# Kernel tuning notes

Hardware: AMD Instinct MI355X
Metric: run time of the kernel (lower is better)

## Reference

```python
import jax, jax.numpy as jnp
import numpy as np

BINS = 32
MAX_DIST = 128
EMB = 1024
DQ = 64
DV = 64
H = 16
B = 8
L = 1024


def _t5_bucket_table():
    # matches: clamp(n,max=m) + (log(clamp(n,min=m)-m+1)*(bins-1-m)/log(max_distance-m+1)).long()
    n = np.arange(MAX_DIST + 1)
    m = BINS // 2
    idx = np.minimum(n, m) + (
        np.log(np.maximum(n, m) - m + 1) * (BINS - 1 - m) / np.log(MAX_DIST - m + 1)
    ).astype(np.int64)
    return jnp.asarray(idx)


def setup_inputs() -> dict:
    key = jax.random.key(0)
    ks = jax.random.split(key, 8)
    s = 0.02
    return {
        "x": jax.random.normal(ks[0], (B, L, EMB), dtype=jnp.float32),
        "qk_w": jax.random.normal(ks[1], (2 * DQ * H, EMB), dtype=jnp.float32) * s,
        "qk_b": jnp.zeros((2 * DQ * H,), dtype=jnp.float32),
        "v_w": jax.random.normal(ks[2], (DV * H, EMB), dtype=jnp.float32) * s,
        "v_b": jnp.zeros((DV * H,), dtype=jnp.float32),
        "out_w": jax.random.normal(ks[3], (EMB, DV * H), dtype=jnp.float32) * s,
        "out_b": jnp.zeros((EMB,), dtype=jnp.float32),
        "bias": jax.random.normal(ks[4], (BINS, H), dtype=jnp.float32) * s,  # causal -> bins rows
    }


def reference(x, qk_w, qk_b, v_w, v_b, out_w, out_b, bias):
    # projections
    qk = (x @ qk_w.T + qk_b).reshape(B, L, H, 2 * DQ).transpose(0, 2, 1, 3)  # [B,H,L,2DQ]
    q, k = qk[..., :DQ], qk[..., DQ:]
    v = (x @ v_w.T + v_b).reshape(B, L, H, DV).transpose(0, 2, 1, 3)  # [B,H,L,DV]

    # T5 relative-position bias (causal): gather per (i-j) distance bucket
    idx_tab = _t5_bucket_table()
    shifts = jnp.arange(L)[:, None] - jnp.arange(L)[None, :]  # [L,L], i - j
    bins_idx = idx_tab[jnp.clip(jnp.abs(shifts), 0, MAX_DIST)]  # [L,L]
    bmat = bias[bins_idx].transpose(2, 0, 1)  # [H,L,L]
    bmat = jnp.where(shifts < 0, -jnp.inf, bmat)  # causal mask (j > i)

    scale = 1.0 / np.sqrt(DQ).astype(np.float32)
    scores = jnp.einsum("bhid,bhjd->bhij", q, k) * scale + bmat  # [B,H,L,L]
    attn = jax.nn.softmax(scores, axis=-1)
    out = jnp.einsum("bhij,bhjd->bhid", attn, v)  # [B,H,L,DV]
    out = out.transpose(0, 2, 1, 3).reshape(B, L, H * DV)
    return out @ out_w.T + out_b
```

## Files before the change

kernel.cpp:

```cpp
#include <hip/hip_runtime.h>
#include <cmath>


typedef _Float16 f16x8 __attribute__((ext_vector_type(8)));
typedef _Float16 f16x4 __attribute__((ext_vector_type(4)));
typedef float    f32x4 __attribute__((ext_vector_type(4)));

#define NEG_INF (-__builtin_inff())
#define LOG2E 1.4426950408889634f

#if __has_builtin(__builtin_amdgcn_exp2f)
#define EXP2(x) __builtin_amdgcn_exp2f(x)
#else
#define EXP2(x) exp2f(x)
#endif

__device__ __forceinline__ void gl_lds16(const void* g, void* l) {
  __builtin_amdgcn_global_load_lds(
      (__attribute__((address_space(1))) void*)g,
      (__attribute__((address_space(3))) void*)l,
      16, 0, 0);
}

__device__ __forceinline__ f32x4 mfma32(f16x8 a, f16x8 b, f32x4 c) {
  return __builtin_amdgcn_mfma_f32_16x16x32_f16(a, b, c, 0, 0, 0);
}
__device__ __forceinline__ f32x4 mfma16(f16x4 a, f16x4 b, f32x4 c) {
  return __builtin_amdgcn_mfma_f32_16x16x16f16(a, b, c, 0, 0, 0);
}

__global__ void cvt_kernel(const float* __restrict__ in,
                           _Float16* __restrict__ out, int n4) {
  int i = blockIdx.x * blockDim.x + threadIdx.x;
  if (i >= n4) return;
  float4 v = reinterpret_cast<const float4*>(in)[i];
  f16x4 o;
  o[0] = (_Float16)v.x; o[1] = (_Float16)v.y;
  o[2] = (_Float16)v.z; o[3] = (_Float16)v.w;
  reinterpret_cast<f16x4*>(out)[i] = o;
}

template <int MODE>
__global__ __launch_bounds__(256, 4) void gemm_kernel(
    const _Float16* __restrict__ A, const _Float16* __restrict__ Bm,
    int M, int N, int K,
    const float* __restrict__ bias_q, const float* __restrict__ bias_v,
    _Float16* __restrict__ qkbuf, _Float16* __restrict__ vtbuf,
    const float* __restrict__ bias_o, float* __restrict__ outf) {
  __shared__ __align__(16) _Float16 lds_a[2][128 * 32];
  __shared__ __align__(16) _Float16 lds_b[2][128 * 32];
  const int t = threadIdx.x;
  const int w = t >> 6;
  const int lane = t & 63;
  const int lq = lane & 15, lg = lane >> 4;
  const int wr = w >> 1, wc = w & 1;
  const int m0 = blockIdx.y * 128, n0 = blockIdx.x * 128;

  const _Float16* pA0 = A + (size_t)(m0 + (t >> 2)) * K + (t & 3) * 8;
  const _Float16* pA1 = pA0 + (size_t)64 * K;
  const _Float16* pB0 = Bm + (size_t)(n0 + (t >> 2)) * K + (t & 3) * 8;
  const _Float16* pB1 = pB0 + (size_t)64 * K;
  const int wofs = w * 512;

#define GEMM_STAGE(buf, kk)                      \
  do {                                           \
    gl_lds16(pA0 + (kk), &lds_a[buf][wofs]);     \
    gl_lds16(pA1 + (kk), &lds_a[buf][2048 + wofs]); \
    gl_lds16(pB0 + (kk), &lds_b[buf][wofs]);     \
    gl_lds16(pB1 + (kk), &lds_b[buf][2048 + wofs]); \
  } while (0)

#define GEMM_COMPUTE(buf)                                                    \
  do {                                                                       \
    f16x8 af[4], bfr[4];                                                     \
    _Pragma("unroll") for (int mi = 0; mi < 4; ++mi) af[mi] =                \
        *(const f16x8*)&lds_a[buf][(wr * 64 + mi * 16 + lq) * 32 + lg * 8];  \
    _Pragma("unroll") for (int ni = 0; ni < 4; ++ni) bfr[ni] =               \
        *(const f16x8*)&lds_b[buf][(wc * 64 + ni * 16 + lq) * 32 + lg * 8];  \
    __builtin_amdgcn_s_setprio(1);                                           \
    _Pragma("unroll") for (int mi = 0; mi < 4; ++mi)                         \
        _Pragma("unroll") for (int ni = 0; ni < 4; ++ni) acc[mi][ni] =       \
            mfma32(af[mi], bfr[ni], acc[mi][ni]);                            \
    __builtin_amdgcn_s_setprio(0);                                           \
  } while (0)

  f32x4 acc[4][4];
#pragma unroll
  for (int mi = 0; mi < 4; ++mi)
#pragma unroll
    for (int ni = 0; ni < 4; ++ni) acc[mi][ni] = (f32x4){0.f, 0.f, 0.f, 0.f};

  GEMM_STAGE(0, 0);

  int cur = 0;
  for (int k0 = 0; k0 < K - 32; k0 += 32) {
    const int nx = cur ^ 1;
    GEMM_STAGE(nx, k0 + 32);
    asm volatile("s_waitcnt vmcnt(4)" ::: "memory");
    __builtin_amdgcn_s_barrier();
    asm volatile("" ::: "memory");
    GEMM_COMPUTE(cur);
    asm volatile("" ::: "memory");
    __builtin_amdgcn_s_barrier();
    cur = nx;
  }
  asm volatile("s_waitcnt vmcnt(0)" ::: "memory");
  __builtin_amdgcn_s_barrier();
  asm volatile("" ::: "memory");
  GEMM_COMPUTE(cur);
#undef GEMM_STAGE
#undef GEMM_COMPUTE

  if (MODE == 0) {
    const bool isqk = (n0 < 2048);
#pragma unroll
    for (int mi = 0; mi < 4; ++mi)
#pragma unroll
      for (int ni = 0; ni < 4; ++ni)
#pragma unroll
        for (int r = 0; r < 4; ++r) {
          const int mg = m0 + wr * 64 + mi * 16 + lg * 4 + r;
          const int ng = n0 + wc * 64 + ni * 16 + lq;
          const int bb = mg >> 10, ii = mg & 1023;
          float val = acc[mi][ni][r];
          if (isqk) {
            val += bias_q[ng];
            const int hh = ng >> 7, cc = ng & 127;
            qkbuf[((size_t)((bb * 16 + hh) * 1024 + ii)) * 128 + cc] =
                (_Float16)val;
          } else {
            const int nn = ng - 2048;
            val += bias_v[nn];
            const int hh = nn >> 6, dv = nn & 63;
            vtbuf[((size_t)((bb * 16 + hh) * 64 + dv)) * 1024 + ii] =
                (_Float16)val;
          }
        }
  } else {
#pragma unroll
    for (int mi = 0; mi < 4; ++mi)
#pragma unroll
      for (int ni = 0; ni < 4; ++ni)
#pragma unroll
        for (int r = 0; r < 4; ++r) {
          const int mg = m0 + wr * 64 + mi * 16 + lg * 4 + r;
          const int ng = n0 + wc * 64 + ni * 16 + lq;
          outf[(size_t)mg * N + ng] = acc[mi][ni][r] + bias_o[ng];
        }
  }
}

__device__ __forceinline__ void stage_kv(const _Float16* __restrict__ kb,
                                         const _Float16* __restrict__ vtb,
                                         int j0, _Float16* kl, _Float16* vl,
                                         int t) {
  const int r0 = t >> 3, c0 = t & 7;
  const int r1 = r0 + 32;
  const int kc0 = c0 ^ (r0 & 7), kc1 = c0 ^ (r1 & 7);
  gl_lds16(kb + (size_t)(j0 + r0) * 128 + kc0 * 8, kl + t * 8);
  gl_lds16(kb + (size_t)(j0 + r1) * 128 + kc1 * 8, kl + (t + 256) * 8);
  gl_lds16(vtb + (size_t)r0 * 1024 + j0 + kc0 * 8, vl + t * 8);
  gl_lds16(vtb + (size_t)r1 * 1024 + j0 + kc1 * 8, vl + (t + 256) * 8);
}

__device__ __forceinline__ void softmax16(f32x4 (&st)[4], f16x4 (&ph)[4],
                                          int qi, int j0, bool far,
                                          const float* __restrict__ tab,
                                          float t128, int lg4, float& m_run,
                                          float& l_part, f32x4 (&oacc)[4]) {
  float xs[16];
  float lmax = NEG_INF;
  if (far) {
#pragma unroll
    for (int js = 0; js < 4; ++js)
#pragma unroll
      for (int r = 0; r < 4; ++r) {
        const float xv = fmaf(st[js][r], 0.125f * LOG2E, t128);
        xs[js * 4 + r] = xv;
        lmax = fmaxf(lmax, xv);
      }
  } else {
#pragma unroll
    for (int js = 0; js < 4; ++js)
#pragma unroll
      for (int r = 0; r < 4; ++r) {
        const int jj = j0 + js * 16 + lg4 + r;
        const int dd = qi - jj;
        const int idx = dd < 0 ? 0 : (dd > 128 ? 128 : dd);
        const float xv =
            (dd < 0) ? NEG_INF : fmaf(st[js][r], 0.125f * LOG2E, tab[idx]);
        xs[js * 4 + r] = xv;
        lmax = fmaxf(lmax, xv);
      }
  }
  if (__any(lmax > m_run + 8.0f)) {
    float tmax = fmaxf(lmax, __shfl_xor(lmax, 16));
    tmax = fmaxf(tmax, __shfl_xor(tmax, 32));
    const float m_new = fmaxf(m_run, tmax);
    const float sf = EXP2(m_run - m_new);
    m_run = m_new;
    l_part *= sf;
    f32x4 sfv;
#pragma unroll
    for (int r = 0; r < 4; ++r) sfv[r] = __shfl(sf, lg4 + r);
#pragma unroll
    for (int db = 0; db < 4; ++db) oacc[db] *= sfv;
  }
  float ls = 0.f;
#pragma unroll
  for (int js = 0; js < 4; ++js)
#pragma unroll
    for (int r = 0; r < 4; ++r) {
      const float p = EXP2(xs[js * 4 + r] - m_run);
      ls += p;
      ph[js][r] = (_Float16)p;
    }
  l_part += ls;
}

__global__ __launch_bounds__(256, 4) void attn_kernel(
    const _Float16* __restrict__ qk,
    const _Float16* __restrict__ vt,
    const float* __restrict__ bias,
    _Float16* __restrict__ ao) {
  __shared__ __align__(16) _Float16 kls[2][64 * 64];
  __shared__ __align__(16) _Float16 vls[2][64 * 64];
  __shared__ float tab[132];
  const int t = threadIdx.x;
  const int bid = blockIdx.x;
  const int bh = (bid & 7) * 16 + (bid >> 6);
  const int b4 = (bid >> 3) & 7;
  const int h = bh & 15, b = bh >> 4;
  if (t < 129) {
    const int bucket =
        (t <= 16) ? t : 16 + (int)(log((double)(t - 15)) * 15.0 / log(113.0));
    tab[t] = bias[bucket * 16 + h] * LOG2E;
  }

  const int w = t >> 6, lane = t & 63;
  const int lq = lane & 15, lg = lane >> 4;
  const int lg4 = lg * 4, lg8 = lg * 8;
  const int tA = b4, tB = 15 - b4;
  const int q0A = tA * 64 + w * 16, q0B = tB * 64 + w * 16;
  const int qA = q0A + lq, qB = q0B + lq;
  const _Float16* qkb = qk + (size_t)bh * 1024 * 128;
  const _Float16* kb = qkb + 64;
  const _Float16* vtb = vt + (size_t)bh * 64 * 1024;

  const f16x8 qfA0 = *(const f16x8*)&qkb[qA * 128 + lg8];
  const f16x8 qfA1 = *(const f16x8*)&qkb[qA * 128 + 32 + lg8];
  const f16x8 qfB0 = *(const f16x8*)&qkb[qB * 128 + lg8];
  const f16x8 qfB1 = *(const f16x8*)&qkb[qB * 128 + 32 + lg8];

  f32x4 oA[4], oB[4];
#pragma unroll
  for (int db = 0; db < 4; ++db) {
    oA[db] = (f32x4){0.f, 0.f, 0.f, 0.f};
    oB[db] = (f32x4){0.f, 0.f, 0.f, 0.f};
  }
  float mA = NEG_INF, lAp = 0.f, mB = NEG_INF, lBp = 0.f;

  stage_kv(kb, vtb, 0, kls[0], vls[0], t);
  __syncthreads();
  const float t128 = tab[128];
  const int krsw = lq & 7;
  const int vsw = (lq & 7) << 1;
  int cur = 0;

  for (int jt = 0; jt <= tB; ++jt) {
    const int j0 = jt * 64;
    if (jt < tB) stage_kv(kb, vtb, j0 + 64, kls[cur ^ 1], vls[cur ^ 1], t);
    const bool aact = (jt <= tA);
    const _Float16* kbf = kls[cur];
    const _Float16* vbf = vls[cur];

    f32x4 stA[4], stB[4];
#pragma unroll
    for (int js = 0; js < 4; ++js) {
      const int rowb = (js * 16 + lq) * 64;
      const f16x8 kf0 = *(const f16x8*)&kbf[rowb + ((lg ^ krsw) << 3)];
      const f16x8 kf1 = *(const f16x8*)&kbf[rowb + (((lg + 4) ^ krsw) << 3)];
      if (aact) {
        stA[js] = mfma32(kf0, qfA0, (f32x4){0.f, 0.f, 0.f, 0.f});
        stA[js] = mfma32(kf1, qfA1, stA[js]);
      }
      stB[js] = mfma32(kf0, qfB0, (f32x4){0.f, 0.f, 0.f, 0.f});
      stB[js] = mfma32(kf1, qfB1, stB[js]);
    }

    f16x4 phA[4], phB[4];
    if (aact)
      softmax16(stA, phA, qA, j0, q0A - j0 >= 192, tab, t128, lg4, mA, lAp,
                oA);
    softmax16(stB, phB, qB, j0, q0B - j0 >= 192, tab, t128, lg4, mB, lBp, oB);

#pragma unroll
    for (int js = 0; js < 4; ++js)
#pragma unroll
      for (int db = 0; db < 4; ++db) {
        const f16x4 vf = *(const f16x4*)&vbf[(db * 16 + lq) * 64 +
                                             ((((js << 2) + lg) ^ vsw) << 2)];
        if (aact) oA[db] = mfma16(phA[js], vf, oA[db]);
        oB[db] = mfma16(phB[js], vf, oB[db]);
      }

    __syncthreads();
    cur ^= 1;
  }

  _Float16* aob = ao + ((size_t)b * 1024) * 1024 + h * 64;
  {
    float lt = lAp + __shfl_xor(lAp, 16);
    lt += __shfl_xor(lt, 32);
    f32x4 linv;
#pragma unroll
    for (int r = 0; r < 4; ++r) linv[r] = 1.0f / __shfl(lt, lg4 + r);
#pragma unroll
    for (int db = 0; db < 4; ++db)
#pragma unroll
      for (int r = 0; r < 4; ++r)
        aob[(size_t)(q0A + lg4 + r) * 1024 + db * 16 + lq] =
            (_Float16)(oA[db][r] * linv[r]);
  }
  {
    float lt = lBp + __shfl_xor(lBp, 16);
    lt += __shfl_xor(lt, 32);
    f32x4 linv;
#pragma unroll
    for (int r = 0; r < 4; ++r) linv[r] = 1.0f / __shfl(lt, lg4 + r);
#pragma unroll
    for (int db = 0; db < 4; ++db)
#pragma unroll
      for (int r = 0; r < 4; ++r)
        aob[(size_t)(q0B + lg4 + r) * 1024 + db * 16 + lq] =
            (_Float16)(oB[db][r] * linv[r]);
  }
}

extern "C" void kernel_launch(void* const* d_in, const int* in_sizes, int n_in,
                              void* d_out, int out_size, void* d_ws,
                              size_t ws_size, hipStream_t stream) {
  const float* x = (const float*)d_in[0];
  const float* qk_w = (const float*)d_in[1];
  const float* qk_b = (const float*)d_in[2];
  const float* v_w = (const float*)d_in[3];
  const float* v_b = (const float*)d_in[4];
  const float* out_w = (const float*)d_in[5];
  const float* out_b = (const float*)d_in[6];
  const float* bias = (const float*)d_in[7];
  float* out = (float*)d_out;

  _Float16* xb = (_Float16*)d_ws;
  _Float16* wb = xb + (size_t)8388608;
  _Float16* owb = wb + (size_t)3145728;
  _Float16* qkbuf = owb + (size_t)1048576;
  _Float16* vtbuf = qkbuf + (size_t)16777216;
  _Float16* ao = vtbuf + (size_t)8388608;

  cvt_kernel<<<8192, 256, 0, stream>>>(x, xb, 2097152);
  cvt_kernel<<<2048, 256, 0, stream>>>(qk_w, wb, 524288);
  cvt_kernel<<<1024, 256, 0, stream>>>(v_w, wb + 2097152, 262144);
  cvt_kernel<<<1024, 256, 0, stream>>>(out_w, owb, 262144);

  gemm_kernel<0><<<dim3(24, 64), 256, 0, stream>>>(
      xb, wb, 8192, 3072, 1024, qk_b, v_b, qkbuf, vtbuf, nullptr, nullptr);

  attn_kernel<<<1024, 256, 0, stream>>>(qkbuf, vtbuf, bias, ao);

  gemm_kernel<1><<<dim3(8, 64), 256, 0, stream>>>(
      ao, owb, 8192, 1024, 1024, nullptr, nullptr, nullptr, nullptr, out_b, out);
}
```

Before: 194.2 us.

## Rewrite GEMM main loop with inline ds_read, XCD-aware block swizzle, unroll by two

The projection GEMM kernel now remaps block indices with a modulo-8 swizzle so that neighbouring tiles land on the same XCD and share L2. The double-buffered k-loop is unrolled by two with precomputed LDS base addresses, and fragments are read with inline-asm ds_read_b128 instructions using immediate offsets, followed by an explicit lgkmcnt wait and a scheduling barrier before the MFMAs. Launch bounds drop from 4 to 3 waves-per-EU to give the compiler more registers. The aim is less address arithmetic and better L2 locality. The risks are lower occupancy, and an explicit swizzle that assumes the block count is divisible by 8.

```diff
diff --git a/kernel.cpp b/kernel.cpp
--- a/kernel.cpp
+++ b/kernel.cpp
@@ -28,6 +28,8 @@
 __device__ __forceinline__ f32x4 mfma16(f16x4 a, f16x4 b, f32x4 c) {
   return __builtin_amdgcn_mfma_f32_16x16x16f16(a, b, c, 0, 0, 0);
 }
+
+typedef __attribute__((address_space(3))) _Float16* lds_f16p;
 
 __global__ void cvt_kernel(const float* __restrict__ in,
                            _Float16* __restrict__ out, int n4) {
@@ -40,8 +42,42 @@
   reinterpret_cast<f16x4*>(out)[i] = o;
 }
 
+#define GEMM_VM4 asm volatile("s_waitcnt vmcnt(4)" ::: "memory")
+#define GEMM_VM0 asm volatile("s_waitcnt vmcnt(0)" ::: "memory")
+#define GEMM_BAR __builtin_amdgcn_s_barrier()
+#define DSR(d, a, o) \
+  asm volatile("ds_read_b128 %0, %1 offset:" o : "=v"(d) : "v"(a))
+
+#define GEMM_STAGE(buf, kk)                         \
+  do {                                              \
+    gl_lds16(pA0 + (kk), &lds_a[buf][wofs]);        \
+    gl_lds16(pA1 + (kk), &lds_a[buf][2048 + wofs]); \
+    gl_lds16(pB0 + (kk), &lds_b[buf][wofs]);        \
+    gl_lds16(pB1 + (kk), &lds_b[buf][2048 + wofs]); \
+  } while (0)
+
+#define GEMM_COMPUTE(aB, bB)                                     \
+  do {                                                           \
+    f16x8 af[4], bf[4];                                          \
+    DSR(af[0], aB, "0");                                         \
+    DSR(af[1], aB, "1024");                                      \
+    DSR(af[2], aB, "2048");                                      \
+    DSR(af[3], aB, "3072");                                      \
+    DSR(bf[0], bB, "0");                                         \
+    DSR(bf[1], bB, "1024");                                      \
+    DSR(bf[2], bB, "2048");                                      \
+    DSR(bf[3], bB, "3072");                                      \
+    asm volatile("s_waitcnt lgkmcnt(0)" ::: "memory");           \
+    __builtin_amdgcn_sched_barrier(0);                           \
+    __builtin_amdgcn_s_setprio(1);                               \
+    _Pragma("unroll") for (int mi = 0; mi < 4; ++mi)             \
+        _Pragma("unroll") for (int ni = 0; ni < 4; ++ni)         \
+            acc[mi][ni] = mfma32(af[mi], bf[ni], acc[mi][ni]);   \
+    __builtin_amdgcn_s_setprio(0);                               \
+  } while (0)
+
 template <int MODE>
-__global__ __launch_bounds__(256, 4) void gemm_kernel(
+__global__ __launch_bounds__(256, 3) void gemm_kernel(
     const _Float16* __restrict__ A, const _Float16* __restrict__ Bm,
     int M, int N, int K,
     const float* __restrict__ bias_q, const float* __restrict__ bias_v,
@@ -54,7 +90,13 @@
   const int lane = t & 63;
   const int lq = lane & 15, lg = lane >> 4;
   const int wr = w >> 1, wc = w & 1;
-  const int m0 = blockIdx.y * 128, n0 = blockIdx.x * 128;
+
+  const int ngx = gridDim.x;
+  const int nwg = ngx * gridDim.y;
+  const int f = blockIdx.x + blockIdx.y * ngx;
+  const int swz = (f & 7) * (nwg >> 3) + (f >> 3);
+  const int bx = swz % ngx, by = swz / ngx;
+  const int m0 = by * 128, n0 = bx * 128;
 
   const _Float16* pA0 = A + (size_t)(m0 + (t >> 2)) * K + (t & 3) * 8;
   const _Float16* pA1 = pA0 + (size_t)64 * K;
@@ -62,27 +104,12 @@
   const _Float16* pB1 = pB0 + (size_t)64 * K;
   const int wofs = w * 512;
 
-#define GEMM_STAGE(buf, kk)                      \
-  do {                                           \
-    gl_lds16(pA0 + (kk), &lds_a[buf][wofs]);     \
-    gl_lds16(pA1 + (kk), &lds_a[buf][2048 + wofs]); \
-    gl_lds16(pB0 + (kk), &lds_b[buf][wofs]);     \
-    gl_lds16(pB1 + (kk), &lds_b[buf][2048 + wofs]); \
-  } while (0)
-
-#define GEMM_COMPUTE(buf)                                                    \
-  do {                                                                       \
-    f16x8 af[4], bfr[4];                                                     \
-    _Pragma("unroll") for (int mi = 0; mi < 4; ++mi) af[mi] =                \
-        *(const f16x8*)&lds_a[buf][(wr * 64 + mi * 16 + lq) * 32 + lg * 8];  \
-    _Pragma("unroll") for (int ni = 0; ni < 4; ++ni) bfr[ni] =               \
-        *(const f16x8*)&lds_b[buf][(wc * 64 + ni * 16 + lq) * 32 + lg * 8];  \
-    __builtin_amdgcn_s_setprio(1);                                           \
-    _Pragma("unroll") for (int mi = 0; mi < 4; ++mi)                         \
-        _Pragma("unroll") for (int ni = 0; ni < 4; ++ni) acc[mi][ni] =       \
-            mfma32(af[mi], bfr[ni], acc[mi][ni]);                            \
-    __builtin_amdgcn_s_setprio(0);                                           \
-  } while (0)
+  const uint32_t aB0 = (uint32_t)(uintptr_t)(lds_f16p)&lds_a[0][0] +
+                       (uint32_t)((wr * 64 + lq) * 64 + lg * 16);
+  const uint32_t aB1 = aB0 + 8192;
+  const uint32_t bB0 = (uint32_t)(uintptr_t)(lds_f16p)&lds_b[0][0] +
+                       (uint32_t)((wc * 64 + lq) * 64 + lg * 16);
+  const uint32_t bB1 = bB0 + 8192;
 
   f32x4 acc[4][4];
 #pragma unroll
@@ -91,25 +118,26 @@
     for (int ni = 0; ni < 4; ++ni) acc[mi][ni] = (f32x4){0.f, 0.f, 0.f, 0.f};
 
   GEMM_STAGE(0, 0);
-
-  int cur = 0;
-  for (int k0 = 0; k0 < K - 32; k0 += 32) {
-    const int nx = cur ^ 1;
-    GEMM_STAGE(nx, k0 + 32);
-    asm volatile("s_waitcnt vmcnt(4)" ::: "memory");
-    __builtin_amdgcn_s_barrier();
-    asm volatile("" ::: "memory");
-    GEMM_COMPUTE(cur);
-    asm volatile("" ::: "memory");
-    __builtin_amdgcn_s_barrier();
-    cur = nx;
-  }
-  asm volatile("s_waitcnt vmcnt(0)" ::: "memory");
-  __builtin_amdgcn_s_barrier();
-  asm volatile("" ::: "memory");
-  GEMM_COMPUTE(cur);
-#undef GEMM_STAGE
-#undef GEMM_COMPUTE
+  for (int kt = 0; kt < K - 64; kt += 64) {
+    GEMM_STAGE(1, kt + 32);
+    GEMM_VM4;
+    GEMM_BAR;
+    GEMM_COMPUTE(aB0, bB0);
+    GEMM_BAR;
+    GEMM_STAGE(0, kt + 64);
+    GEMM_VM4;
+    GEMM_BAR;
+    GEMM_COMPUTE(aB1, bB1);
+    GEMM_BAR;
+  }
+  GEMM_STAGE(1, K - 32);
+  GEMM_VM4;
+  GEMM_BAR;
+  GEMM_COMPUTE(aB0, bB0);
+  GEMM_BAR;
+  GEMM_VM0;
+  GEMM_BAR;
+  GEMM_COMPUTE(aB1, bB1);
 
   if (MODE == 0) {
     const bool isqk = (n0 < 2048);
```

New measurement: 184.6 us. 1.05x faster.
